# Kernel tuning notes

Hardware: AMD Instinct MI355X
Metric: run time of the kernel (lower is better)

## Reference

```python
import jax, jax.numpy as jnp
import numpy as np

FORMULA_OH_SIZES = [20, 20, 20, 20, 20]
SPECT_BIN_N = 512


def layer_norm(x, g, b, eps=1e-5):
    m = jnp.mean(x, axis=-1, keepdims=True)
    v = jnp.var(x, axis=-1, keepdims=True)
    return (x - m) * jax.lax.rsqrt(v + eps) * g + b


def gru_cell(x, h, W_ih, W_hh, b_ih, b_hh):
    # torch.nn.GRUCell math
    gi = x @ W_ih.T + b_ih
    gh = h @ W_hh.T + b_hh
    i_r, i_z, i_n = jnp.split(gi, 3, axis=-1)
    h_r, h_z, h_n = jnp.split(gh, 3, axis=-1)
    r = jax.nn.sigmoid(i_r + h_r)
    z = jax.nn.sigmoid(i_z + h_z)
    n = jnp.tanh(i_n + r * h_n)
    return (1.0 - z) * n + z * h


def structured_one_hot(x, sizes, accum=True):
    # x: [N, len(sizes)] integer element counts -> concatenated (accumulated) one-hots
    outs = []
    for i, s in enumerate(sizes):
        v = jnp.clip(x[:, i].astype(jnp.int32), 0, s - 1)
        if accum:
            oh = (jnp.arange(s)[None, :] <= v[:, None]).astype(jnp.float32)  # thermometer
        else:
            oh = jax.nn.one_hot(v, s, dtype=jnp.float32)
        outs.append(oh)
    return jnp.concatenate(outs, axis=-1)


def setup_inputs():
    key = jax.random.key(0)
    ks = jax.random.split(key, 16)
    B, A, GF, HW, S, M = 16, 32, 128, 4, 4096, 8
    G = GF * HW                       # 512 = g_feat_in * highway_steps_n
    FE = sum(FORMULA_OH_SIZES)        # 100
    D = 512                           # internal_d
    vert_feat_in = jax.random.normal(ks[0], (B, A, GF, HW), jnp.float32)
    vert_mask_in = jnp.ones((B, A), jnp.float32)
    elem_id = jax.random.randint(ks[1], (B, A), 0, 5)
    vert_element_oh = jax.nn.one_hot(elem_id, 5, dtype=jnp.float32)
    adj_oh = jnp.zeros((B, A, A, 4), jnp.float32)  # unused by forward
    atom_subsets = jax.random.bernoulli(ks[2], 0.5, (B, S, A)).astype(jnp.float32)
    masses = jax.random.uniform(ks[3], (B, S, M), jnp.float32, 0.0, SPECT_BIN_N - 1.0)
    intens = jax.random.uniform(ks[4], (B, S, M), jnp.float32)
    atom_subsets_peaks = jnp.stack([masses, intens], axis=-1)

    def lin(k, o, i):
        return (jax.random.normal(k, (o, i), jnp.float32) / np.sqrt(i)).astype(jnp.float32)

    return dict(
        vert_feat_in=vert_feat_in, vert_mask_in=vert_mask_in,
        vert_element_oh=vert_element_oh, adj_oh=adj_oh,
        atom_subsets=atom_subsets, atom_subsets_peaks=atom_subsets_peaks,
        ln_sub_g=jnp.ones((G,), jnp.float32), ln_sub_b=jnp.zeros((G,), jnp.float32),
        W_ih=lin(ks[5], 3 * G, FE), W_hh=lin(ks[6], 3 * G, G),
        b_ih=jnp.zeros((3 * G,), jnp.float32), b_hh=jnp.zeros((3 * G,), jnp.float32),
        W1=lin(ks[7], D, G), b1=jnp.zeros((D,), jnp.float32),
        W2a=lin(ks[8], D, D), b2a=jnp.zeros((D,), jnp.float32),
        W2b=lin(ks[9], D, D), b2b=jnp.zeros((D,), jnp.float32),
        ln_pre_g=jnp.ones((D,), jnp.float32), ln_pre_b=jnp.zeros((D,), jnp.float32),
        Ws=lin(ks[10], 1, D), bs=jnp.zeros((1,), jnp.float32),
    )


def reference(vert_feat_in, vert_mask_in, vert_element_oh, adj_oh, atom_subsets,
              atom_subsets_peaks, ln_sub_g, ln_sub_b, W_ih, W_hh, b_ih, b_hh,
              W1, b1, W2a, b2a, W2b, b2b, ln_pre_g, ln_pre_b, Ws, bs):
    B, A, GF, HW = vert_feat_in.shape
    S = atom_subsets.shape[1]
    vf = vert_feat_in.reshape(B, A, GF * HW)                       # [B,A,G]
    masked_vf = vf * vert_mask_in[:, :, None]
    subs_m = atom_subsets * vert_mask_in[:, None, :]               # [B,S,A]
    swvs = jnp.einsum('bag,bsa->bsg', masked_vf, subs_m)           # [B,S,G]
    # per-subset element counts -> structured one-hot formula encoding
    counts = jnp.einsum('bae,bsa->bse', vert_element_oh, atom_subsets).astype(jnp.int32)
    pf_flat = structured_one_hot(counts.reshape(B * S, -1), FORMULA_OH_SIZES, accum=True)
    subset_size = jnp.sum(subs_m, axis=2) + 1e-4                   # [B,S]
    mean = swvs / subset_size[:, :, None]
    normed = layer_norm(mean, ln_sub_g, ln_sub_b)                  # [B,S,G]
    h = gru_cell(pf_flat, normed.reshape(B * S, -1), W_ih, W_hh, b_ih, b_hh)
    h = h.reshape(normed.shape)
    x = jax.nn.relu(h @ W1.T + b1)
    x = jax.nn.relu(x @ W2a.T + b2a)
    x = jax.nn.relu(x @ W2b.T + b2b)   # (extra F.relu in original is idempotent)
    x = layer_norm(x, ln_pre_g, ln_pre_b)
    scores = (x @ Ws.T + bs)[..., 0]                               # [B,S]
    probs = jax.nn.softmax(scores, axis=-1)
    # mass histogram: scatter intensity*prob into rounded-mass bins
    masses = atom_subsets_peaks[..., 0]                            # [B,S,M]
    intens = atom_subsets_peaks[..., 1]
    bins = jnp.clip(jnp.round(masses).astype(jnp.int32), 0, SPECT_BIN_N - 1)
    contrib = intens * probs[:, :, None]                           # [B,S,M]
    spect = jnp.zeros((B, SPECT_BIN_N), x.dtype).at[
        jnp.arange(B)[:, None], bins.reshape(B, -1)].add(contrib.reshape(B, -1))
    return (spect, probs)
```

## Files before the change

kernel.cpp:

```cpp
#include <hip/hip_runtime.h>
#include <math.h>

#define B_ 16
#define A_ 32
#define G_ 512
#define S_ 4096
#define M_ 8
#define BS_ 65536
#define KC_ 640
#define NG_ 1536
#define SMH 16384

typedef _Float16 half8 __attribute__((ext_vector_type(8)));
typedef _Float16 half4v __attribute__((ext_vector_type(4)));
typedef _Float16 half2v __attribute__((ext_vector_type(2)));
typedef float floatx4 __attribute__((ext_vector_type(4)));

typedef const __attribute__((address_space(1))) void* gas_t;
typedef __attribute__((address_space(3))) void* las_t;

__device__ __forceinline__ float wave_sum_f(float v){
#pragma unroll
  for (int o = 32; o > 0; o >>= 1) v += __shfl_xor(v, o);
  return v;
}
__device__ __forceinline__ float wave_max_f(float v){
#pragma unroll
  for (int o = 32; o > 0; o >>= 1) v = fmaxf(v, __shfl_xor(v, o));
  return v;
}
__device__ __forceinline__ float sigmoidf_(float x){ return 1.f/(1.f+__expf(-x)); }
__device__ __forceinline__ float tanhf_(float x){ return 1.f - 2.f/(__expf(2.f*x)+1.f); }

__global__ __launch_bounds__(256) void k_cvtw(const float* __restrict__ s0,
                                              const float* __restrict__ s1,
                                              const float* __restrict__ s2,
                                              _Float16* __restrict__ d,
                                              const float* __restrict__ Whh,
                                              const float* __restrict__ Wih,
                                              _Float16* __restrict__ Wcat){
  if (blockIdx.y == 3){
    int j0 = blockIdx.x*6;
    for (int j = j0; j < j0+6; ++j)
      for (int p = threadIdx.x; p < KC_; p += 256){
        float v = 0.f;
        if (p < 512) v = Whh[(size_t)j*512 + p];
        else if (p < 612) v = Wih[(size_t)j*100 + (p - 512)];
        Wcat[(size_t)j*KC_ + p] = (_Float16)v;
      }
    return;
  }
  const float* s = (blockIdx.y == 0) ? s0 : (blockIdx.y == 1) ? s1 : s2;
  int i = (blockIdx.x*256 + threadIdx.x)*4;
  if (i >= G_*G_) return;
  float4 v = *(const float4*)(s+i);
  half4v o; o[0]=(_Float16)v.x; o[1]=(_Float16)v.y; o[2]=(_Float16)v.z; o[3]=(_Float16)v.w;
  *(half4v*)(d + (size_t)blockIdx.y*G_*G_ + i) = o;
}

__global__ __launch_bounds__(256) void k_prep_mfma(
    const float* __restrict__ vf, const float* __restrict__ mask,
    const float* __restrict__ eoh, const float* __restrict__ subs,
    const float* __restrict__ ln_g, const float* __restrict__ ln_b,
    _Float16* __restrict__ Abuf){
  __shared__ _Float16 s_mvfT[G_*A_];
  __shared__ _Float16 s_sm[128*A_];
  __shared__ float s_m[A_];
  __shared__ float s_e[A_*5];
  __shared__ float s_ssum[128];
  __shared__ float s_red1[2][4][16];
  __shared__ float s_red2[2][4][16];
  int tid = threadIdx.x;
  int bx = blockIdx.x, b = blockIdx.y;
  int lane = tid & 63, w = tid >> 6;
  int q = lane >> 4, l15 = lane & 15;
  size_t row0 = (size_t)b*S_ + (size_t)bx*128;
  if (tid < A_)   s_m[tid] = mask[b*A_ + tid];
  if (tid < A_*5) s_e[tid] = eoh[b*A_*5 + tid];
  __syncthreads();
  {
    int p = tid & 15, gseg = tid >> 4;
    float mk0 = s_m[2*p], mk1 = s_m[2*p+1];
    const float* v0 = vf + ((size_t)b*A_ + 2*p)*G_ + gseg*32;
    const float* v1 = v0 + G_;
#pragma unroll
    for (int i = 0; i < 32; i += 4){
      float4 a = *(const float4*)(v0 + i);
      float4 c = *(const float4*)(v1 + i);
      float av[4] = {a.x, a.y, a.z, a.w};
      float cv[4] = {c.x, c.y, c.z, c.w};
#pragma unroll
      for (int j = 0; j < 4; ++j){
        half2v h; h[0] = (_Float16)(av[j]*mk0); h[1] = (_Float16)(cv[j]*mk1);
        *(half2v*)(s_mvfT + (gseg*32 + i + j)*A_ + 2*p) = h;
      }
    }
  }
  {
    int s = tid >> 1, hh = tid & 1;
    const float* sp = subs + (row0 + s)*A_ + hh*16;
    _Float16* dst = s_sm + s*A_ + hh*16;
#pragma unroll
    for (int i = 0; i < 16; i += 4){
      float4 v = *(const float4*)(sp + i);
      half4v h; h[0]=(_Float16)v.x; h[1]=(_Float16)v.y; h[2]=(_Float16)v.z; h[3]=(_Float16)v.w;
      *(half4v*)(dst + i) = h;
    }
  }
  __syncthreads();
  if (tid < 128){
    int s = tid;
    float ssum = 0.f, c0=0.f, c1=0.f, c2=0.f, c3=0.f, c4=0.f;
#pragma unroll
    for (int a = 0; a < A_; ++a){
      float v = (float)s_sm[s*A_ + a];
      ssum += v * s_m[a];
      c0 += v * s_e[a*5+0]; c1 += v * s_e[a*5+1]; c2 += v * s_e[a*5+2];
      c3 += v * s_e[a*5+3]; c4 += v * s_e[a*5+4];
    }
    int cc[5];
    cc[0] = min(max((int)(c0+0.5f),0),19); cc[1] = min(max((int)(c1+0.5f),0),19);
    cc[2] = min(max((int)(c2+0.5f),0),19); cc[3] = min(max((int)(c3+0.5f),0),19);
    cc[4] = min(max((int)(c4+0.5f),0),19);
    s_ssum[s] = ssum;
    _Float16* dst = Abuf + (row0 + s)*KC_ + 512;
#pragma unroll
    for (int t = 0; t < 16; ++t){
      half8 hv;
#pragma unroll
      for (int u = 0; u < 8; ++u){
        int k = t*8 + u;
        float v = 0.f;
        if (k < 100){ int f = k/20, l = k - f*20; v = (l <= cc[f]) ? 1.f : 0.f; }
        hv[u] = (_Float16)v;
      }
      *(half8*)(dst + t*8) = hv;
    }
  }
  half8 bf[8]; float lng[8], lnb[8];
#pragma unroll
  for (int t = 0; t < 8; ++t){
    int g = w*128 + t*16 + l15;
    bf[t] = *(const half8*)(s_mvfT + g*A_ + q*8);
    lng[t] = ln_g[g]; lnb[t] = ln_b[g];
  }
  __syncthreads();
  _Float16* s_stage = s_mvfT;
  for (int gi = 0; gi < 8; ++gi){
    half8 af = *(const half8*)(s_sm + (gi*16 + l15)*A_ + q*8);
    floatx4 c[8];
#pragma unroll
    for (int t = 0; t < 8; ++t){
      floatx4 z = {0.f, 0.f, 0.f, 0.f};
      c[t] = __builtin_amdgcn_mfma_f32_16x16x32_f16(af, bf[t], z, 0, 0, 0);
    }
    float p1[4] = {0.f,0.f,0.f,0.f}, p2[4] = {0.f,0.f,0.f,0.f};
#pragma unroll
    for (int t = 0; t < 8; ++t)
#pragma unroll
      for (int r = 0; r < 4; ++r){ float v = c[t][r]; p1[r] += v; p2[r] += v*v; }
#pragma unroll
    for (int off = 1; off < 16; off <<= 1)
#pragma unroll
      for (int r = 0; r < 4; ++r){
        p1[r] += __shfl_xor(p1[r], off);
        p2[r] += __shfl_xor(p2[r], off);
      }
    int gb = gi & 1;
    if (l15 == 0){
#pragma unroll
      for (int r = 0; r < 4; ++r){ s_red1[gb][w][q*4+r] = p1[r]; s_red2[gb][w][q*4+r] = p2[r]; }
    }
    __syncthreads();
#pragma unroll
    for (int r = 0; r < 4; ++r){
      int sl = gi*16 + q*4 + r;
      int rr = q*4 + r;
      float t1 = s_red1[gb][0][rr] + s_red1[gb][1][rr] + s_red1[gb][2][rr] + s_red1[gb][3][rr];
      float t2 = s_red2[gb][0][rr] + s_red2[gb][1][rr] + s_red2[gb][2][rr] + s_red2[gb][3][rr];
      float inv = 1.f/(s_ssum[sl] + 1e-4f);
      float mu = t1*inv*(1.f/512.f);
      float var = t2*inv*inv*(1.f/512.f) - mu*mu;
      float rs = rsqrtf(var + 1e-5f);
      _Float16* srow = s_stage + (q*4 + r)*528;
#pragma unroll
      for (int t = 0; t < 8; ++t){
        float o = (c[t][r]*inv - mu)*rs*lng[t] + lnb[t];
        srow[w*128 + t*16 + l15] = (_Float16)o;
      }
    }
    __syncthreads();
#pragma unroll
    for (int k = 0; k < 4; ++k){
      int v = tid + k*256;
      int row = v >> 6, c8 = (v & 63)*8;
      *(half8*)(Abuf + (row0 + gi*16 + row)*KC_ + c8) =
          *(const half8*)(s_stage + row*528 + c8);
    }
  }
}

__global__ __launch_bounds__(512) void k_gru_fused(
    const _Float16* __restrict__ Abuf, const _Float16* __restrict__ Wcat,
    const float* __restrict__ bih, const float* __restrict__ bhh,
    _Float16* __restrict__ H){
  __shared__ _Float16 smA[2][128*32];
  __shared__ _Float16 smB[2][192*32];
  int tid = threadIdx.x;
  int lane = tid & 63, wvid = tid >> 6;
  int wm = wvid & 1, wn = wvid >> 1;
  int q = lane >> 4, l15 = lane & 15;
  int mt = blockIdx.x*64 + (blockIdx.y >> 3);
  int dt = blockIdx.y & 7;
  int m0 = mt*128, n0 = dt*64;
  floatx4 acc[3][4] = {};
  floatx4 accNI[4] = {};
  int offA[4], offB[3];
#pragma unroll
  for (int i = 0; i < 4; ++i){
    int r = wm*64 + i*16 + l15;
    offA[i] = (r*4 + (q ^ ((r>>2)&3)))*8;
  }
#pragma unroll
  for (int g = 0; g < 3; ++g){
    int rb = g*64 + wn*16 + l15;
    offB[g] = (rb*4 + (q ^ ((rb>>2)&3)))*8;
  }
  const _Float16* gA;
  {
    int u = wvid*64 + lane;
    int r = u >> 2, c = (u & 3) ^ ((r >> 2) & 3);
    gA = Abuf + (size_t)(m0 + r)*KC_ + c*8;
  }
  const _Float16* gB0;
  {
    int u = wvid*64 + lane;
    int rb = u >> 2, c = (u & 3) ^ ((rb >> 2) & 3);
    int grow = (rb >> 6)*512 + n0 + (rb & 63);
    gB0 = Wcat + (size_t)grow*KC_ + c*8;
  }
  const _Float16* gB1 = nullptr;
  if (wvid < 4){
    int u = (8 + wvid)*64 + lane;
    int rb = u >> 2, c = (u & 3) ^ ((rb >> 2) & 3);
    int grow = (rb >> 6)*512 + n0 + (rb & 63);
    gB1 = Wcat + (size_t)grow*KC_ + c*8;
  }
  __builtin_amdgcn_global_load_lds((gas_t)gA,  (las_t)(smA[0] + wvid*512), 16, 0, 0);
  __builtin_amdgcn_global_load_lds((gas_t)gB0, (las_t)(smB[0] + wvid*512), 16, 0, 0);
  if (wvid < 4)
    __builtin_amdgcn_global_load_lds((gas_t)gB1, (las_t)(smB[0] + (8+wvid)*512), 16, 0, 0);
  asm volatile("s_waitcnt vmcnt(0)");
  __builtin_amdgcn_s_barrier();
  const int NT = KC_/32;
  for (int t = 0; t < NT; ++t){
    int cur = t & 1;
    if (t + 1 < NT){
      int kc = (t+1)*32;
      __builtin_amdgcn_global_load_lds((gas_t)(gA + kc),  (las_t)(smA[cur^1] + wvid*512), 16, 0, 0);
      __builtin_amdgcn_global_load_lds((gas_t)(gB0 + kc), (las_t)(smB[cur^1] + wvid*512), 16, 0, 0);
      if (wvid < 4)
        __builtin_amdgcn_global_load_lds((gas_t)(gB1 + kc), (las_t)(smB[cur^1] + (8+wvid)*512), 16, 0, 0);
    }
    half8 af[4], bfv[3];
#pragma unroll
    for (int i = 0; i < 4; ++i) af[i] = *(const half8*)(smA[cur] + offA[i]);
#pragma unroll
    for (int g = 0; g < 3; ++g) bfv[g] = *(const half8*)(smB[cur] + offB[g]);
    if (t < 16){
#pragma unroll
      for (int g = 0; g < 3; ++g)
#pragma unroll
        for (int i = 0; i < 4; ++i)
          acc[g][i] = __builtin_amdgcn_mfma_f32_16x16x32_f16(af[i], bfv[g], acc[g][i], 0, 0, 0);
    } else {
#pragma unroll
      for (int i = 0; i < 4; ++i){
        acc[0][i] = __builtin_amdgcn_mfma_f32_16x16x32_f16(af[i], bfv[0], acc[0][i], 0, 0, 0);
        acc[1][i] = __builtin_amdgcn_mfma_f32_16x16x32_f16(af[i], bfv[1], acc[1][i], 0, 0, 0);
        accNI[i]  = __builtin_amdgcn_mfma_f32_16x16x32_f16(af[i], bfv[2], accNI[i], 0, 0, 0);
      }
    }
    asm volatile("s_waitcnt vmcnt(0)");
    __builtin_amdgcn_s_barrier();
  }
  int d = n0 + wn*16 + l15;
  float br  = bih[d] + bhh[d];
  float bz  = bih[512+d] + bhh[512+d];
  float bnh = bhh[1024+d];
  float bni = bih[1024+d];
#pragma unroll
  for (int i = 0; i < 4; ++i){
#pragma unroll
    for (int r = 0; r < 4; ++r){
      int m = m0 + wm*64 + i*16 + q*4 + r;
      float gr  = acc[0][i][r] + br;
      float gz  = acc[1][i][r] + bz;
      float hn  = acc[2][i][r] + bnh;
      float in_ = accNI[i][r] + bni;
      float rrv = sigmoidf_(gr);
      float zz  = sigmoidf_(gz);
      float nn  = tanhf_(in_ + rrv*hn);
      float hp  = (float)Abuf[(size_t)m*KC_ + d];
      H[(size_t)m*G_ + d] = (_Float16)((1.f-zz)*nn + zz*hp);
    }
  }
}

#define STG_A8(T) do{ \
    __builtin_amdgcn_global_load_lds((gas_t)(pA0 + (T)*64),           (las_t)(&smA8[(T)&1][0] + wvid*1024),        16, 0, 0); \
    __builtin_amdgcn_global_load_lds((gas_t)(pA1 + (T)*64),           (las_t)(&smA8[(T)&1][0] + wvid*1024 + 512),  16, 0, 0); \
    __builtin_amdgcn_global_load_lds((gas_t)(pA0 + 128*G_ + (T)*64),  (las_t)(&smA8[(T)&1][0] + 8192 + wvid*1024), 16, 0, 0); \
    __builtin_amdgcn_global_load_lds((gas_t)(pA1 + 128*G_ + (T)*64),  (las_t)(&smA8[(T)&1][0] + 8192 + wvid*1024 + 512), 16, 0, 0); \
  }while(0)
#define STG_B8(T,H) do{ \
    __builtin_amdgcn_global_load_lds((gas_t)(pB0 + (H)*128*G_ + (T)*64), (las_t)(&smB8[(T)&1][0] + (H)*8192 + wvid*1024),       16, 0, 0); \
    __builtin_amdgcn_global_load_lds((gas_t)(pB1 + (H)*128*G_ + (T)*64), (las_t)(&smB8[(T)&1][0] + (H)*8192 + wvid*1024 + 512), 16, 0, 0); \
  }while(0)
#define RD_A8(DST, T, MF0) do{ \
    const _Float16* ba_ = &smA8[(T)&1][0]; \
    DST[0][0] = *(const half8*)(ba_ + aoff0 + (MF0)*1024); \
    DST[0][1] = *(const half8*)(ba_ + aoff1 + (MF0)*1024); \
    DST[1][0] = *(const half8*)(ba_ + aoff0 + ((MF0)+1)*1024); \
    DST[1][1] = *(const half8*)(ba_ + aoff1 + ((MF0)+1)*1024); \
  }while(0)
#define RD_B8(DST, T) do{ \
    const _Float16* bb_ = &smB8[(T)&1][0]; \
    _Pragma("unroll") \
    for (int nf_ = 0; nf_ < 4; ++nf_){ \
      DST[nf_][0] = *(const half8*)(bb_ + boff0 + nf_*1024); \
      DST[nf_][1] = *(const half8*)(bb_ + boff1 + nf_*1024); \
    } \
  }while(0)
#define MMQ8(AV, BV, MF0) do{ \
    _Pragma("unroll") \
    for (int u_ = 0; u_ < 2; ++u_) \
    _Pragma("unroll") \
    for (int nf_ = 0; nf_ < 4; ++nf_){ \
      acc[(MF0)+u_][nf_] = __builtin_amdgcn_mfma_f32_16x16x32_f16(AV[u_][0], BV[nf_][0], acc[(MF0)+u_][nf_], 0, 0, 0); \
      acc[(MF0)+u_][nf_] = __builtin_amdgcn_mfma_f32_16x16x32_f16(AV[u_][1], BV[nf_][1], acc[(MF0)+u_][nf_], 0, 0, 0); \
    } \
  }while(0)
#define PH_Q0(T, BC) do{ if ((T)+1 <= 7) STG_A8((T)+1); RD_A8(a_o, T, 2); \
    __builtin_amdgcn_s_barrier(); __builtin_amdgcn_s_setprio(1); MMQ8(a_e, BC, 0); \
    __builtin_amdgcn_s_setprio(0); __builtin_amdgcn_s_barrier(); }while(0)
#define PH_Q1(T, BC) do{ if ((T)+2 <= 7) STG_B8((T)+2, 0); RD_A8(a_e, T, 4); \
    __builtin_amdgcn_s_barrier(); __builtin_amdgcn_s_setprio(1); MMQ8(a_o, BC, 2); \
    __builtin_amdgcn_s_setprio(0); __builtin_amdgcn_s_barrier(); }while(0)
#define PH_Q2(T, BC) do{ if ((T)+2 <= 7) STG_B8((T)+2, 1); RD_A8(a_o, T, 6); \
    __builtin_amdgcn_s_barrier(); __builtin_amdgcn_s_setprio(1); MMQ8(a_e, BC, 4); \
    __builtin_amdgcn_s_setprio(0); __builtin_amdgcn_s_barrier(); }while(0)
#define PH_Q3(T, BC, BN) do{ \
    if ((T) < 7){ \
      if ((T) < 6) asm volatile("s_waitcnt vmcnt(4)" ::: "memory"); \
      else         asm volatile("s_waitcnt vmcnt(0)" ::: "memory"); \
      RD_B8(BN, (T)+1); RD_A8(a_e, (T)+1, 0); \
    } \
    __builtin_amdgcn_s_barrier(); __builtin_amdgcn_s_setprio(1); MMQ8(a_o, BC, 6); \
    __builtin_amdgcn_s_setprio(0); __builtin_amdgcn_s_barrier(); }while(0)
#define TILE8(T, BC, BN) do{ PH_Q0(T, BC); PH_Q1(T, BC); PH_Q2(T, BC); PH_Q3(T, BC, BN); }while(0)

#define K8_SETUP(Amat, Wmat) \
  int tid = threadIdx.x; \
  int lane = tid & 63, wvid = tid >> 6; \
  int wm = wvid & 1, wn = wvid >> 1; \
  int q = lane >> 4, l15 = lane & 15; \
  int x_ = l15 & 7; \
  int bid = blockIdx.x; \
  int wg = (bid & 7)*64 + (bid >> 3); \
  int mt = wg >> 1, nt = wg & 1; \
  int m0 = mt*256, n0 = nt*256; \
  int swzlo = (q ^ (x_ & 3))*8; \
  int aoff0 = (wm*128 + l15)*64 + ((0 ^ (x_>>2))*4)*8 + swzlo; \
  int aoff1 = (wm*128 + l15)*64 + ((1 ^ (x_>>2))*4)*8 + swzlo; \
  int boff0 = (wn*64 + l15)*64 + ((0 ^ (x_>>2))*4)*8 + swzlo; \
  int boff1 = (wn*64 + l15)*64 + ((1 ^ (x_>>2))*4)*8 + swzlo; \
  int srow = wvid*16 + (lane >> 3); \
  int sc = ((lane & 7) ^ ((lane >> 3) & 7))*8; \
  const _Float16* pA0 = Amat + (size_t)(m0 + srow)*G_ + sc; \
  const _Float16* pA1 = Amat + (size_t)(m0 + srow + 8)*G_ + sc; \
  const _Float16* pB0 = Wmat + (size_t)(n0 + srow)*G_ + sc; \
  const _Float16* pB1 = Wmat + (size_t)(n0 + srow + 8)*G_ + sc; \
  floatx4 acc[8][4] = {}; \
  half8 a_e[2][2], a_o[2][2], bA[4][2], bB[4][2]; \
  STG_A8(0); STG_B8(0,0); STG_B8(0,1); STG_B8(1,0); STG_B8(1,1); \
  asm volatile("s_waitcnt vmcnt(4)" ::: "memory"); \
  __builtin_amdgcn_s_barrier(); \
  RD_B8(bA, 0); RD_A8(a_e, 0, 0); \
  TILE8(0, bA, bB); TILE8(1, bB, bA); \
  TILE8(2, bA, bB); TILE8(3, bB, bA); \
  TILE8(4, bA, bB); TILE8(5, bB, bA); \
  TILE8(6, bA, bB); TILE8(7, bB, bA);

__global__ __launch_bounds__(512, 2) void k_gemm8(
    const _Float16* __restrict__ A, const _Float16* __restrict__ W,
    const float* __restrict__ bias, _Float16* __restrict__ Out){
  __shared__ _Float16 smA8[2][SMH];
  __shared__ _Float16 smB8[2][SMH];
  K8_SETUP(A, W)
  float bv[4];
#pragma unroll
  for (int nf = 0; nf < 4; ++nf) bv[nf] = bias[n0 + wn*64 + nf*16 + l15];
#pragma unroll
  for (int mf = 0; mf < 8; ++mf){
    int m = m0 + wm*128 + mf*16 + q*4;
#pragma unroll
    for (int nf = 0; nf < 4; ++nf){
      int n = n0 + wn*64 + nf*16 + l15;
#pragma unroll
      for (int r = 0; r < 4; ++r)
        Out[(size_t)(m+r)*G_ + n] = (_Float16)fmaxf(acc[mf][nf][r] + bv[nf], 0.f);
    }
  }
}

__global__ __launch_bounds__(512, 2) void k_ff38(
    const _Float16* __restrict__ A, const _Float16* __restrict__ W,
    const float* __restrict__ bias, const float* __restrict__ ln_pre_g,
    const float* __restrict__ Ws, float* __restrict__ Pbuf){
  __shared__ _Float16 smA8[2][SMH];
  __shared__ _Float16 smB8[2][SMH];
  K8_SETUP(A, W)
  float gws[4], bv[4];
#pragma unroll
  for (int nf = 0; nf < 4; ++nf){
    int n = n0 + wn*64 + nf*16 + l15;
    gws[nf] = ln_pre_g[n]*Ws[n];
    bv[nf] = bias[n];
  }
  float* sP = (float*)&smB8[0][0];
#pragma unroll
  for (int mf = 0; mf < 8; ++mf){
#pragma unroll
    for (int r = 0; r < 4; ++r){
      float p1 = 0.f, p2 = 0.f, p3 = 0.f;
#pragma unroll
      for (int nf = 0; nf < 4; ++nf){
        float xv = fmaxf(acc[mf][nf][r] + bv[nf], 0.f);
        p1 += xv; p2 += xv*xv; p3 += gws[nf]*xv;
      }
#pragma unroll
      for (int off = 1; off < 16; off <<= 1){
        p1 += __shfl_xor(p1, off);
        p2 += __shfl_xor(p2, off);
        p3 += __shfl_xor(p3, off);
      }
      if (l15 == 0){
        int rl = wm*128 + mf*16 + q*4 + r;
        sP[(rl*4 + wn)*3 + 0] = p1;
        sP[(rl*4 + wn)*3 + 1] = p2;
        sP[(rl*4 + wn)*3 + 2] = p3;
      }
    }
  }
  __syncthreads();
  if (tid < 256){
    int m = m0 + tid;
    float* dst = Pbuf + ((size_t)m*2 + nt)*3;
#pragma unroll
    for (int c = 0; c < 3; ++c)
      dst[c] = sP[(tid*4+0)*3+c] + sP[(tid*4+1)*3+c] +
               sP[(tid*4+2)*3+c] + sP[(tid*4+3)*3+c];
  }
}

__global__ __launch_bounds__(256) void k_score_fin(
    const float* __restrict__ Pbuf, const float* __restrict__ g,
    const float* __restrict__ bta, const float* __restrict__ Ws,
    const float* __restrict__ bs, float* __restrict__ scores,
    float* __restrict__ spect){
  __shared__ float red[8];
  int tid = threadIdx.x, lane = tid & 63, wv = tid >> 6;
  if (blockIdx.x < 32) spect[(size_t)blockIdx.x*256 + tid] = 0.f;
  int i0 = tid*2;
  float c1p = g[i0]*Ws[i0] + g[i0+1]*Ws[i0+1];
  float c2p = bta[i0]*Ws[i0] + bta[i0+1]*Ws[i0+1];
  c1p = wave_sum_f(c1p); c2p = wave_sum_f(c2p);
  if (lane == 0){ red[wv] = c1p; red[4+wv] = c2p; }
  __syncthreads();
  float c1 = red[0]+red[1]+red[2]+red[3];
  float c2 = red[4]+red[5]+red[6]+red[7] + bs[0];
  size_t row = (size_t)blockIdx.x*256 + tid;
  const float* p = Pbuf + row*6;
  float2 u0 = *(const float2*)p;
  float2 u1 = *(const float2*)(p+2);
  float2 u2 = *(const float2*)(p+4);
  float P1 = u0.x + u1.y;
  float P2 = u0.y + u2.x;
  float P3 = u1.x + u2.y;
  float mu = P1*(1.f/512.f);
  float var = P2*(1.f/512.f) - mu*mu;
  float rs = rsqrtf(var + 1e-5f);
  scores[row] = rs*(P3 - mu*c1) + c2;
}

__global__ __launch_bounds__(1024) void k_softmax(
    const float* __restrict__ scores, float* __restrict__ probs){
  __shared__ float red[16];
  int b = blockIdx.x, tid = threadIdx.x, lane = tid & 63, wv = tid >> 6;
  const float* sp = scores + (size_t)b*S_;
  float* pp = probs + (size_t)b*S_;
  float mx = -1e30f;
  for (int i = tid; i < S_; i += 1024) mx = fmaxf(mx, sp[i]);
  mx = wave_max_f(mx);
  if (lane == 0) red[wv] = mx;
  __syncthreads();
  float m2 = red[0];
#pragma unroll
  for (int k = 1; k < 16; ++k) m2 = fmaxf(m2, red[k]);
  __syncthreads();
  float sum = 0.f;
  for (int i = tid; i < S_; i += 1024){
    float e = __expf(sp[i]-m2);
    pp[i] = e;
    sum += e;
  }
  sum = wave_sum_f(sum);
  if (lane == 0) red[wv] = sum;
  __syncthreads();
  float s2 = 0.f;
#pragma unroll
  for (int k = 0; k < 16; ++k) s2 += red[k];
  float inv = 1.f/s2;
  for (int i = tid; i < S_; i += 1024)
    pp[i] *= inv;
}

__global__ __launch_bounds__(256) void k_spect_p(
    const float* __restrict__ peaks, const float* __restrict__ probs,
    float* __restrict__ spect){
  __shared__ float bins[512];
  int b = blockIdx.x, chunk = blockIdx.y, tid = threadIdx.x;
  bins[tid] = 0.f; bins[tid+256] = 0.f;
  __syncthreads();
  int s0 = chunk*(S_/8);
  for (int i = tid; i < (S_/8)*M_; i += 256){
    int s = s0 + (i >> 3), m = i & 7;
    const float* pk = peaks + (((size_t)b*S_ + s)*M_ + m)*2;
    float mass = pk[0], inten = pk[1];
    float p = probs[(size_t)b*S_ + s];
    int bin = (int)rintf(mass);
    bin = min(max(bin, 0), 511);
    atomicAdd(&bins[bin], inten*p);
  }
  __syncthreads();
  atomicAdd(&spect[(size_t)b*512 + tid],       bins[tid]);
  atomicAdd(&spect[(size_t)b*512 + tid + 256], bins[tid+256]);
}

extern "C" void kernel_launch(void* const* d_in, const int* in_sizes, int n_in,
                              void* d_out, int out_size, void* d_ws, size_t ws_size,
                              hipStream_t stream) {
  const float* vf       = (const float*)d_in[0];
  const float* mask     = (const float*)d_in[1];
  const float* eoh      = (const float*)d_in[2];
  const float* subs     = (const float*)d_in[4];
  const float* peaks    = (const float*)d_in[5];
  const float* ln_sub_g = (const float*)d_in[6];
  const float* ln_sub_b = (const float*)d_in[7];
  const float* W_ih     = (const float*)d_in[8];
  const float* W_hh     = (const float*)d_in[9];
  const float* b_ih     = (const float*)d_in[10];
  const float* b_hh     = (const float*)d_in[11];
  const float* W1       = (const float*)d_in[12];
  const float* b1       = (const float*)d_in[13];
  const float* W2a      = (const float*)d_in[14];
  const float* b2a      = (const float*)d_in[15];
  const float* W2b      = (const float*)d_in[16];
  const float* b2b      = (const float*)d_in[17];
  const float* ln_pre_g = (const float*)d_in[18];
  const float* ln_pre_b = (const float*)d_in[19];
  const float* Ws       = (const float*)d_in[20];
  const float* bs       = (const float*)d_in[21];
  float* out = (float*)d_out;
  float* probs_out = out + (size_t)B_*512;

  char* w = (char*)d_ws;
  float* scores = (float*)w;     w += (size_t)BS_*4;
  float* Pbuf   = (float*)w;     w += (size_t)BS_*12*4;
  _Float16* Wcat = (_Float16*)w; w += (size_t)NG_*KC_*2;
  _Float16* W1h  = (_Float16*)w; w += (size_t)G_*G_*2;
  _Float16* W2ah = (_Float16*)w; w += (size_t)G_*G_*2;
  _Float16* W2bh = (_Float16*)w; w += (size_t)G_*G_*2;
  _Float16* Abuf = (_Float16*)w; w += (size_t)BS_*KC_*2;
  _Float16* bufh0 = (_Float16*)w;
  _Float16* bufh1 = Abuf;

  k_cvtw<<<dim3(256, 4), 256, 0, stream>>>(W1, W2a, W2b, W1h, W_hh, W_ih, Wcat);
  k_prep_mfma<<<dim3(S_/128, B_), 256, 0, stream>>>(vf, mask, eoh, subs,
                                                    ln_sub_g, ln_sub_b, Abuf);
  k_gru_fused<<<dim3(8, 512), 512, 0, stream>>>(Abuf, Wcat, b_ih, b_hh, bufh0);
  k_gemm8<<<512, 512, 0, stream>>>(bufh0, W1h,  b1,  bufh1);
  k_gemm8<<<512, 512, 0, stream>>>(bufh1, W2ah, b2a, bufh0);
  k_ff38<<<512, 512, 0, stream>>>(bufh0, W2bh, b2b, ln_pre_g, Ws, Pbuf);
  k_score_fin<<<BS_/256, 256, 0, stream>>>(Pbuf, ln_pre_g, ln_pre_b, Ws, bs,
                                           scores, out);
  k_softmax<<<B_, 1024, 0, stream>>>(scores, probs_out);
  k_spect_p<<<dim3(B_, 8), 256, 0, stream>>>(peaks, probs_out, out);
}
```

Before: 473.7 us.

## Fuse score, softmax and spectrum into one tail kernel; split prep blocks

Merges the score finalization, per-batch softmax and mass-histogram scatter into a single kernel with one 1024-thread block per batch. Scores and probabilities stay in registers and shared memory, which removes two launches and the global round trips for scores and probs. The prep kernel now launches twice as many blocks with 64 rows each, raising parallelism at the cost of recomputing the transposed vertex features per block. The histogram loop now runs on only 16 blocks, so less parallel work is available for the scatter.

```diff
diff --git a/kernel.cpp b/kernel.cpp
--- a/kernel.cpp
+++ b/kernel.cpp
@@ -64,17 +64,17 @@
     const float* __restrict__ ln_g, const float* __restrict__ ln_b,
     _Float16* __restrict__ Abuf){
   __shared__ _Float16 s_mvfT[G_*A_];
-  __shared__ _Float16 s_sm[128*A_];
+  __shared__ _Float16 s_sm[64*A_];
   __shared__ float s_m[A_];
   __shared__ float s_e[A_*5];
-  __shared__ float s_ssum[128];
+  __shared__ float s_ssum[64];
   __shared__ float s_red1[2][4][16];
   __shared__ float s_red2[2][4][16];
   int tid = threadIdx.x;
-  int bx = blockIdx.x, b = blockIdx.y;
+  int bx = blockIdx.x, b = blockIdx.y, z = blockIdx.z;
   int lane = tid & 63, w = tid >> 6;
   int q = lane >> 4, l15 = lane & 15;
-  size_t row0 = (size_t)b*S_ + (size_t)bx*128;
+  size_t row0 = (size_t)b*S_ + (size_t)bx*128 + (size_t)z*64;
   if (tid < A_)   s_m[tid] = mask[b*A_ + tid];
   if (tid < A_*5) s_e[tid] = eoh[b*A_*5 + tid];
   __syncthreads();
@@ -97,18 +97,17 @@
     }
   }
   {
-    int s = tid >> 1, hh = tid & 1;
-    const float* sp = subs + (row0 + s)*A_ + hh*16;
-    _Float16* dst = s_sm + s*A_ + hh*16;
-#pragma unroll
-    for (int i = 0; i < 16; i += 4){
-      float4 v = *(const float4*)(sp + i);
-      half4v h; h[0]=(_Float16)v.x; h[1]=(_Float16)v.y; h[2]=(_Float16)v.z; h[3]=(_Float16)v.w;
-      *(half4v*)(dst + i) = h;
-    }
-  }
-  __syncthreads();
-  if (tid < 128){
+    int s = tid >> 2, hq = tid & 3;
+    const float* sp = subs + (row0 + s)*A_ + hq*8;
+    float4 v0 = *(const float4*)(sp);
+    float4 v1 = *(const float4*)(sp + 4);
+    half8 h;
+    h[0]=(_Float16)v0.x; h[1]=(_Float16)v0.y; h[2]=(_Float16)v0.z; h[3]=(_Float16)v0.w;
+    h[4]=(_Float16)v1.x; h[5]=(_Float16)v1.y; h[6]=(_Float16)v1.z; h[7]=(_Float16)v1.w;
+    *(half8*)(s_sm + s*A_ + hq*8) = h;
+  }
+  __syncthreads();
+  if (tid < 64){
     int s = tid;
     float ssum = 0.f, c0=0.f, c1=0.f, c2=0.f, c3=0.f, c4=0.f;
 #pragma unroll
@@ -146,13 +145,13 @@
   }
   __syncthreads();
   _Float16* s_stage = s_mvfT;
-  for (int gi = 0; gi < 8; ++gi){
-    half8 af = *(const half8*)(s_sm + (gi*16 + l15)*A_ + q*8);
+  for (int gl = 0; gl < 4; ++gl){
+    half8 af = *(const half8*)(s_sm + (gl*16 + l15)*A_ + q*8);
     floatx4 c[8];
 #pragma unroll
     for (int t = 0; t < 8; ++t){
-      floatx4 z = {0.f, 0.f, 0.f, 0.f};
-      c[t] = __builtin_amdgcn_mfma_f32_16x16x32_f16(af, bf[t], z, 0, 0, 0);
+      floatx4 zz = {0.f, 0.f, 0.f, 0.f};
+      c[t] = __builtin_amdgcn_mfma_f32_16x16x32_f16(af, bf[t], zz, 0, 0, 0);
     }
     float p1[4] = {0.f,0.f,0.f,0.f}, p2[4] = {0.f,0.f,0.f,0.f};
 #pragma unroll
@@ -166,7 +165,7 @@
         p1[r] += __shfl_xor(p1[r], off);
         p2[r] += __shfl_xor(p2[r], off);
       }
-    int gb = gi & 1;
+    int gb = gl & 1;
     if (l15 == 0){
 #pragma unroll
       for (int r = 0; r < 4; ++r){ s_red1[gb][w][q*4+r] = p1[r]; s_red2[gb][w][q*4+r] = p2[r]; }
@@ -174,7 +173,7 @@
     __syncthreads();
 #pragma unroll
     for (int r = 0; r < 4; ++r){
-      int sl = gi*16 + q*4 + r;
+      int sl = gl*16 + q*4 + r;
       int rr = q*4 + r;
       float t1 = s_red1[gb][0][rr] + s_red1[gb][1][rr] + s_red1[gb][2][rr] + s_red1[gb][3][rr];
       float t2 = s_red2[gb][0][rr] + s_red2[gb][1][rr] + s_red2[gb][2][rr] + s_red2[gb][3][rr];
@@ -194,7 +193,7 @@
     for (int k = 0; k < 4; ++k){
       int v = tid + k*256;
       int row = v >> 6, c8 = (v & 63)*8;
-      *(half8*)(Abuf + (row0 + gi*16 + row)*KC_ + c8) =
+      *(half8*)(Abuf + (row0 + gl*16 + row)*KC_ + c8) =
           *(const half8*)(s_stage + row*528 + c8);
     }
   }
@@ -464,44 +463,53 @@
   }
 }
 
-__global__ __launch_bounds__(256) void k_score_fin(
+__global__ __launch_bounds__(1024) void k_tail(
     const float* __restrict__ Pbuf, const float* __restrict__ g,
     const float* __restrict__ bta, const float* __restrict__ Ws,
-    const float* __restrict__ bs, float* __restrict__ scores,
-    float* __restrict__ spect){
-  __shared__ float red[8];
-  int tid = threadIdx.x, lane = tid & 63, wv = tid >> 6;
-  if (blockIdx.x < 32) spect[(size_t)blockIdx.x*256 + tid] = 0.f;
-  int i0 = tid*2;
-  float c1p = g[i0]*Ws[i0] + g[i0+1]*Ws[i0+1];
-  float c2p = bta[i0]*Ws[i0] + bta[i0+1]*Ws[i0+1];
-  c1p = wave_sum_f(c1p); c2p = wave_sum_f(c2p);
-  if (lane == 0){ red[wv] = c1p; red[4+wv] = c2p; }
-  __syncthreads();
-  float c1 = red[0]+red[1]+red[2]+red[3];
-  float c2 = red[4]+red[5]+red[6]+red[7] + bs[0];
-  size_t row = (size_t)blockIdx.x*256 + tid;
-  const float* p = Pbuf + row*6;
-  float2 u0 = *(const float2*)p;
-  float2 u1 = *(const float2*)(p+2);
-  float2 u2 = *(const float2*)(p+4);
-  float P1 = u0.x + u1.y;
-  float P2 = u0.y + u2.x;
-  float P3 = u1.x + u2.y;
-  float mu = P1*(1.f/512.f);
-  float var = P2*(1.f/512.f) - mu*mu;
-  float rs = rsqrtf(var + 1e-5f);
-  scores[row] = rs*(P3 - mu*c1) + c2;
-}
-
-__global__ __launch_bounds__(1024) void k_softmax(
-    const float* __restrict__ scores, float* __restrict__ probs){
+    const float* __restrict__ bs, const float* __restrict__ peaks,
+    float* __restrict__ spect, float* __restrict__ probs){
   __shared__ float red[16];
+  __shared__ float sprob[S_];
+  __shared__ float bins[512];
   int b = blockIdx.x, tid = threadIdx.x, lane = tid & 63, wv = tid >> 6;
-  const float* sp = scores + (size_t)b*S_;
-  float* pp = probs + (size_t)b*S_;
+  float c1p = 0.f, c2p = 0.f;
+  if (tid < 256){
+    int i0 = tid*2;
+    c1p = g[i0]*Ws[i0] + g[i0+1]*Ws[i0+1];
+    c2p = bta[i0]*Ws[i0] + bta[i0+1]*Ws[i0+1];
+  }
+  c1p = wave_sum_f(c1p);
+  if (lane == 0) red[wv] = c1p;
+  __syncthreads();
+  float c1 = 0.f;
+#pragma unroll
+  for (int k = 0; k < 16; ++k) c1 += red[k];
+  __syncthreads();
+  c2p = wave_sum_f(c2p);
+  if (lane == 0) red[wv] = c2p;
+  __syncthreads();
+  float c2 = bs[0];
+#pragma unroll
+  for (int k = 0; k < 16; ++k) c2 += red[k];
+  __syncthreads();
+  float sc[4];
   float mx = -1e30f;
-  for (int i = tid; i < S_; i += 1024) mx = fmaxf(mx, sp[i]);
+#pragma unroll
+  for (int k = 0; k < 4; ++k){
+    size_t row = (size_t)b*S_ + tid + k*1024;
+    const float* p = Pbuf + row*6;
+    float2 u0 = *(const float2*)p;
+    float2 u1 = *(const float2*)(p+2);
+    float2 u2 = *(const float2*)(p+4);
+    float P1 = u0.x + u1.y;
+    float P2 = u0.y + u2.x;
+    float P3 = u1.x + u2.y;
+    float mu = P1*(1.f/512.f);
+    float var = P2*(1.f/512.f) - mu*mu;
+    float rs = rsqrtf(var + 1e-5f);
+    sc[k] = rs*(P3 - mu*c1) + c2;
+    mx = fmaxf(mx, sc[k]);
+  }
   mx = wave_max_f(mx);
   if (lane == 0) red[wv] = mx;
   __syncthreads();
@@ -510,9 +518,10 @@
   for (int k = 1; k < 16; ++k) m2 = fmaxf(m2, red[k]);
   __syncthreads();
   float sum = 0.f;
-  for (int i = tid; i < S_; i += 1024){
-    float e = __expf(sp[i]-m2);
-    pp[i] = e;
+#pragma unroll
+  for (int k = 0; k < 4; ++k){
+    float e = __expf(sc[k]-m2);
+    sprob[tid + k*1024] = e;
     sum += e;
   }
   sum = wave_sum_f(sum);
@@ -522,30 +531,23 @@
 #pragma unroll
   for (int k = 0; k < 16; ++k) s2 += red[k];
   float inv = 1.f/s2;
-  for (int i = tid; i < S_; i += 1024)
-    pp[i] *= inv;
-}
-
-__global__ __launch_bounds__(256) void k_spect_p(
-    const float* __restrict__ peaks, const float* __restrict__ probs,
-    float* __restrict__ spect){
-  __shared__ float bins[512];
-  int b = blockIdx.x, chunk = blockIdx.y, tid = threadIdx.x;
-  bins[tid] = 0.f; bins[tid+256] = 0.f;
-  __syncthreads();
-  int s0 = chunk*(S_/8);
-  for (int i = tid; i < (S_/8)*M_; i += 256){
-    int s = s0 + (i >> 3), m = i & 7;
+#pragma unroll
+  for (int k = 0; k < 4; ++k){
+    float pv = sprob[tid + k*1024]*inv;
+    sprob[tid + k*1024] = pv;
+    probs[(size_t)b*S_ + tid + k*1024] = pv;
+  }
+  if (tid < 512) bins[tid] = 0.f;
+  __syncthreads();
+  for (int i = tid; i < S_*M_; i += 1024){
+    int s = i >> 3, m = i & 7;
     const float* pk = peaks + (((size_t)b*S_ + s)*M_ + m)*2;
     float mass = pk[0], inten = pk[1];
-    float p = probs[(size_t)b*S_ + s];
-    int bin = (int)rintf(mass);
-    bin = min(max(bin, 0), 511);
-    atomicAdd(&bins[bin], inten*p);
-  }
-  __syncthreads();
-  atomicAdd(&spect[(size_t)b*512 + tid],       bins[tid]);
-  atomicAdd(&spect[(size_t)b*512 + tid + 256], bins[tid+256]);
+    int bin = min(max((int)rintf(mass), 0), 511);
+    atomicAdd(&bins[bin], inten*sprob[s]);
+  }
+  __syncthreads();
+  if (tid < 512) spect[(size_t)b*512 + tid] = bins[tid];
 }
 
 extern "C" void kernel_launch(void* const* d_in, const int* in_sizes, int n_in,
@@ -585,16 +587,15 @@
   _Float16* Abuf = (_Float16*)w; w += (size_t)BS_*KC_*2;
   _Float16* bufh0 = (_Float16*)w;
   _Float16* bufh1 = Abuf;
+  (void)scores;
 
   k_cvtw<<<dim3(256, 4), 256, 0, stream>>>(W1, W2a, W2b, W1h, W_hh, W_ih, Wcat);
-  k_prep_mfma<<<dim3(S_/128, B_), 256, 0, stream>>>(vf, mask, eoh, subs,
-                                                    ln_sub_g, ln_sub_b, Abuf);
+  k_prep_mfma<<<dim3(S_/128, B_, 2), 256, 0, stream>>>(vf, mask, eoh, subs,
+                                                       ln_sub_g, ln_sub_b, Abuf);
   k_gru_fused<<<dim3(8, 512), 512, 0, stream>>>(Abuf, Wcat, b_ih, b_hh, bufh0);
   k_gemm8<<<512, 512, 0, stream>>>(bufh0, W1h,  b1,  bufh1);
   k_gemm8<<<512, 512, 0, stream>>>(bufh1, W2ah, b2a, bufh0);
   k_ff38<<<512, 512, 0, stream>>>(bufh0, W2bh, b2b, ln_pre_g, Ws, Pbuf);
-  k_score_fin<<<BS_/256, 256, 0, stream>>>(Pbuf, ln_pre_g, ln_pre_b, Ws, bs,
-                                           scores, out);
-  k_softmax<<<B_, 1024, 0, stream>>>(scores, probs_out);
-  k_spect_p<<<dim3(B_, 8), 256, 0, stream>>>(peaks, probs_out, out);
-}
+  k_tail<<<B_, 1024, 0, stream>>>(Pbuf, ln_pre_g, ln_pre_b, Ws, bs, peaks,
+                                  out, probs_out);
+}
```

After: 497.9 us. +5.1%, slower.
